# Kernel tuning notes

Hardware: AMD Instinct MI355X
Metric: run time of the kernel (lower is better)

The kernel has to match this reference:

```python
import jax, jax.numpy as jnp
import numpy as np

T, B, I, H, O = 512, 128, 512, 1024, 256

def setup_inputs() -> dict:
    key = jax.random.key(0)
    ks = jax.random.split(key, 7)
    s = 1.0 / np.sqrt(H)
    return {
        "seqs": jax.random.normal(ks[0], (T, B, I), dtype=jnp.float32),
        "W_ih": jax.random.uniform(ks[1], (H, I), minval=-s, maxval=s, dtype=jnp.float32),
        "W_hh": jax.random.uniform(ks[2], (H, H), minval=-s, maxval=s, dtype=jnp.float32),
        "b_ih": jax.random.uniform(ks[3], (H,), minval=-s, maxval=s, dtype=jnp.float32),
        "b_hh": jax.random.uniform(ks[4], (H,), minval=-s, maxval=s, dtype=jnp.float32),
        "W_fc": jax.random.uniform(ks[5], (O, H), minval=-s, maxval=s, dtype=jnp.float32),
        "b_fc": jax.random.uniform(ks[6], (O,), minval=-s, maxval=s, dtype=jnp.float32),
    }

def reference(seqs, W_ih, W_hh, b_ih, b_hh, W_fc, b_fc):
    # Precompute input projections for all timesteps in one big GEMM: [T,B,H]
    x_proj = jnp.einsum('tbi,hi->tbh', seqs, W_ih) + b_ih + b_hh

    def step(h, xp):
        h_new = jax.nn.relu(xp + h @ W_hh.T)
        return h_new, None

    h0 = jnp.zeros((seqs.shape[1], W_hh.shape[0]), dtype=seqs.dtype)
    h_final, _ = jax.lax.scan(step, h0, x_proj)
    return h_final @ W_fc.T + b_fc
```

## Files before the change

### kernel.cpp

```cpp
#include <hip/hip_runtime.h>
#include <hip/hip_bf16.h>
#include <stdint.h>

#define T_STEPS 512
#define BATCH   128
#define IN      512
#define HID     1024
#define OUTN    256

typedef __bf16 bf16x8 __attribute__((ext_vector_type(8)));
typedef float  f32x4  __attribute__((ext_vector_type(4)));
typedef unsigned short us8 __attribute__((ext_vector_type(8)));
typedef unsigned int   ui4 __attribute__((ext_vector_type(4)));

#define TAGM 0x80008000u
#define CLRM 0x7FFF7FFFu

__device__ __forceinline__ unsigned short f2bf(float f) {
    uint32_t u = __float_as_uint(f);
    uint32_t r = (u + 0x7fffu + ((u >> 16) & 1u)) >> 16;
    return (unsigned short)r;
}

__device__ __forceinline__ ui4 ld_u128_agent(const void* p) {
    ui4 v;
    asm volatile("global_load_dwordx4 %0, %1, off sc0 sc1"
                 : "=v"(v) : "v"(p) : "memory");
    return v;
}

__device__ __forceinline__ bf16x8 ld_frag(const unsigned short* smem, int row, int kbyte, int rowstride) {
    int off = row * rowstride + (kbyte ^ ((row & 7) << 4));
    return *reinterpret_cast<const bf16x8*>(reinterpret_cast<const char*>(smem) + off);
}
__device__ __forceinline__ us8 ld_frag_u(const unsigned short* smem, int row, int kbyte, int rowstride) {
    int off = row * rowstride + (kbyte ^ ((row & 7) << 4));
    return *reinterpret_cast<const us8*>(reinterpret_cast<const char*>(smem) + off);
}

__global__ __launch_bounds__(256, 1) void rnn_persistent(
    const float* __restrict__ seqs, const float* __restrict__ W_ih,
    const float* __restrict__ W_hh, const float* __restrict__ b_ih,
    const float* __restrict__ b_hh, const float* __restrict__ W_fc,
    const float* __restrict__ b_fc, float* __restrict__ out,
    unsigned short* __restrict__ hbuf)
{
    const int tid  = threadIdx.x;
    const int lane = tid & 63;
    const int wv   = tid >> 6;
    const int wg   = blockIdx.x;
    const int g    = wg >> 5;
    const int w    = wg & 31;
    const int gr0  = g * 16;
    const int c0   = w * 32;
    const int ln15 = lane & 15;
    const int lk   = lane >> 4;

    __shared__ unsigned short xtile[16 * 512];
    __shared__ unsigned short htile[16 * 1024];
    __shared__ float red[4][16][33];
    __shared__ float biasS[32];

    bf16x8 wih[2][4];
    bf16x8 whh[2][8];
    #pragma unroll
    for (int nt = 0; nt < 2; nt++) {
        const int j = c0 + nt * 16 + ln15;
        #pragma unroll
        for (int s = 0; s < 4; s++) {
            const int k = wv * 128 + s * 32 + lk * 8;
            const float* p = W_ih + j * IN + k;
            us8 u;
            #pragma unroll
            for (int e = 0; e < 8; e++) u[e] = f2bf(p[e]);
            wih[nt][s] = __builtin_bit_cast(bf16x8, u);
        }
        #pragma unroll
        for (int s = 0; s < 8; s++) {
            const int k = wv * 256 + s * 32 + lk * 8;
            const float* p = W_hh + j * HID + k;
            us8 u;
            #pragma unroll
            for (int e = 0; e < 8; e++) u[e] = f2bf(p[e]);
            whh[nt][s] = __builtin_bit_cast(bf16x8, u);
        }
    }
    if (tid < 32) biasS[tid] = b_ih[c0 + tid] + b_hh[c0 + tid];

    int hgoff[8], hloff[8];
    #pragma unroll
    for (int it = 0; it < 8; it++) {
        const int c    = tid + it * 256;
        const int row  = c >> 7;
        const int colc = c & 127;
        hgoff[it] = row * 2048 + colc * 16;
        hloff[it] = row * 2048 + ((colc * 16) ^ ((row & 7) << 4));
    }

    const int xrow[4] = { (tid) >> 6, (tid + 256) >> 6, (tid + 512) >> 6, (tid + 768) >> 6 };
    const int xcol[4] = { (tid) & 63, (tid + 256) & 63, (tid + 512) & 63, (tid + 768) & 63 };

    us8 xbf[4];
    {
        const float* xsrc = seqs + (size_t)gr0 * IN;
        #pragma unroll
        for (int it = 0; it < 4; it++) {
            const float* s4 = xsrc + xrow[it] * IN + xcol[it] * 8;
            float4 a = *reinterpret_cast<const float4*>(s4);
            float4 b = *reinterpret_cast<const float4*>(s4 + 4);
            us8 u;
            u[0]=f2bf(a.x); u[1]=f2bf(a.y); u[2]=f2bf(a.z); u[3]=f2bf(a.w);
            u[4]=f2bf(b.x); u[5]=f2bf(b.y); u[6]=f2bf(b.z); u[7]=f2bf(b.w);
            xbf[it] = u;
        }
    }

    const size_t slotB = (size_t)BATCH * HID * 2;
    char* hbase = reinterpret_cast<char*>(hbuf);

    for (int t = 0; t < T_STEPS; t++) {
        #pragma unroll
        for (int it = 0; it < 4; it++) {
            const int off = xrow[it] * 1024 + ((xcol[it] * 16) ^ ((xrow[it] & 7) << 4));
            *reinterpret_cast<us8*>(reinterpret_cast<char*>(xtile) + off) = xbf[it];
        }
        __syncthreads();

        ui4 hv[8];
        const char* hsrc = hbase + (size_t)(t & 1) * slotB + (size_t)gr0 * HID * 2;
        if (t > 0) {
            #pragma unroll
            for (int it = 0; it < 8; it++) hv[it] = ld_u128_agent(hsrc + hgoff[it]);
        }
        __builtin_amdgcn_sched_barrier(0);

        float4 xr[8];
        {
            const int tn = (t + 1 < T_STEPS) ? t + 1 : t;
            const float* xsrc = seqs + (size_t)tn * (BATCH * IN) + (size_t)gr0 * IN;
            #pragma unroll
            for (int it = 0; it < 4; it++) {
                const float* s4 = xsrc + xrow[it] * IN + xcol[it] * 8;
                xr[2*it]   = *reinterpret_cast<const float4*>(s4);
                xr[2*it+1] = *reinterpret_cast<const float4*>(s4 + 4);
            }
        }
        __builtin_amdgcn_sched_barrier(0);

        f32x4 acc0 = {0.f, 0.f, 0.f, 0.f};
        f32x4 acc1 = {0.f, 0.f, 0.f, 0.f};
        {
            const int kx0b = wv * 256;
            #pragma unroll
            for (int s = 0; s < 4; s++) {
                bf16x8 a = ld_frag(xtile, ln15, kx0b + s * 64 + lk * 16, 1024);
                acc0 = __builtin_amdgcn_mfma_f32_16x16x32_bf16(a, wih[0][s], acc0, 0, 0, 0);
                acc1 = __builtin_amdgcn_mfma_f32_16x16x32_bf16(a, wih[1][s], acc1, 0, 0, 0);
            }
        }

        if (t > 0) {
            const unsigned pr = ((t >> 1) & 1) ? 0x80000000u : 0x00008000u;
            asm volatile("s_waitcnt vmcnt(8)" ::: "memory");
            __builtin_amdgcn_sched_barrier(0);
            unsigned pending = 0xFFu;
            while (true) {
                unsigned np = 0;
                #pragma unroll
                for (int it = 0; it < 8; it++) {
                    if (pending & (1u << it)) {
                        unsigned d = ((hv[it][0] & TAGM) ^ pr) | ((hv[it][1] & TAGM) ^ pr)
                                   | ((hv[it][2] & TAGM) ^ pr) | ((hv[it][3] & TAGM) ^ pr);
                        if (d != 0u) {
                            np |= (1u << it);
                            hv[it] = ld_u128_agent(hsrc + hgoff[it]);
                        }
                    }
                }
                pending = np;
                if (pending == 0u) break;
                asm volatile("s_waitcnt vmcnt(0)" ::: "memory");
                __builtin_amdgcn_sched_barrier(0);
            }
            #pragma unroll
            for (int it = 0; it < 8; it++) {
                ui4 v = hv[it];
                v[0] &= CLRM; v[1] &= CLRM; v[2] &= CLRM; v[3] &= CLRM;
                *reinterpret_cast<ui4*>(reinterpret_cast<char*>(htile) + hloff[it]) = v;
            }
            __syncthreads();

            const int kh0b = wv * 512;
            #pragma unroll
            for (int s = 0; s < 8; s++) {
                bf16x8 a = ld_frag(htile, ln15, kh0b + s * 64 + lk * 16, 2048);
                acc0 = __builtin_amdgcn_mfma_f32_16x16x32_bf16(a, whh[0][s], acc0, 0, 0, 0);
                acc1 = __builtin_amdgcn_mfma_f32_16x16x32_bf16(a, whh[1][s], acc1, 0, 0, 0);
            }
        }

        #pragma unroll
        for (int r = 0; r < 4; r++) {
            red[wv][lk * 4 + r][ln15]      = acc0[r];
            red[wv][lk * 4 + r][16 + ln15] = acc1[r];
        }
        __syncthreads();
        const int hrow = tid >> 4;
        const int co2  = (tid & 15) * 2;
        float v0 = red[0][hrow][co2]   + red[1][hrow][co2]   + red[2][hrow][co2]   + red[3][hrow][co2]   + biasS[co2];
        float v1 = red[0][hrow][co2+1] + red[1][hrow][co2+1] + red[2][hrow][co2+1] + red[3][hrow][co2+1] + biasS[co2+1];
        v0 = fmaxf(v0, 0.0f);
        v1 = fmaxf(v1, 0.0f);

        asm volatile("s_waitcnt vmcnt(0)" ::: "memory");
        __builtin_amdgcn_sched_barrier(0);
        #pragma unroll
        for (int it = 0; it < 4; it++) {
            float4 a = xr[2*it], b = xr[2*it+1];
            us8 u;
            u[0]=f2bf(a.x); u[1]=f2bf(a.y); u[2]=f2bf(a.z); u[3]=f2bf(a.w);
            u[4]=f2bf(b.x); u[5]=f2bf(b.y); u[6]=f2bf(b.z); u[7]=f2bf(b.w);
            xbf[it] = u;
        }

        {
            const unsigned pw = (((t + 1) >> 1) & 1) ? 0x80000000u : 0x00008000u;
            unsigned pack = (unsigned)f2bf(v0) | ((unsigned)f2bf(v1) << 16) | pw;
            unsigned* dst = reinterpret_cast<unsigned*>(
                hbase + (size_t)((t + 1) & 1) * slotB
                + ((size_t)(gr0 + hrow) * HID + c0 + co2) * 2);
            __hip_atomic_store(dst, pack, __ATOMIC_RELAXED, __HIP_MEMORY_SCOPE_AGENT);
        }
    }

    {
        const char* hsrc = hbase + (size_t)gr0 * HID * 2;
        ui4 hv[8];
        #pragma unroll
        for (int it = 0; it < 8; it++) hv[it] = ld_u128_agent(hsrc + hgoff[it]);
        unsigned pending = 0xFFu;
        do {
            asm volatile("s_waitcnt vmcnt(0)" ::: "memory");
            __builtin_amdgcn_sched_barrier(0);
            unsigned np = 0;
            #pragma unroll
            for (int it = 0; it < 8; it++) {
                if (pending & (1u << it)) {
                    unsigned d = ((hv[it][0] & TAGM) ^ 0x00008000u) | ((hv[it][1] & TAGM) ^ 0x00008000u)
                               | ((hv[it][2] & TAGM) ^ 0x00008000u) | ((hv[it][3] & TAGM) ^ 0x00008000u);
                    if (d != 0u) {
                        np |= (1u << it);
                        hv[it] = ld_u128_agent(hsrc + hgoff[it]);
                    }
                }
            }
            pending = np;
        } while (pending);
        #pragma unroll
        for (int it = 0; it < 8; it++) {
            ui4 v = hv[it];
            v[0] &= CLRM; v[1] &= CLRM; v[2] &= CLRM; v[3] &= CLRM;
            *reinterpret_cast<ui4*>(reinterpret_cast<char*>(htile) + hloff[it]) = v;
        }
        __syncthreads();
    }

    {
        const int oi   = tid & 127;
        const int half = tid >> 7;
        const int row  = oi >> 3;
        const int o    = w * 8 + (oi & 7);
        const float* wf = W_fc + (size_t)o * HID + half * 512;
        float sum = 0.f;
        #pragma unroll 4
        for (int ck = 0; ck < 64; ck++) {
            us8 hu = ld_frag_u(htile, row, half * 1024 + ck * 16, 2048);
            float4 wa = *reinterpret_cast<const float4*>(wf + ck * 8);
            float4 wb = *reinterpret_cast<const float4*>(wf + ck * 8 + 4);
            sum += __uint_as_float((unsigned)hu[0] << 16) * wa.x
                 + __uint_as_float((unsigned)hu[1] << 16) * wa.y
                 + __uint_as_float((unsigned)hu[2] << 16) * wa.z
                 + __uint_as_float((unsigned)hu[3] << 16) * wa.w
                 + __uint_as_float((unsigned)hu[4] << 16) * wb.x
                 + __uint_as_float((unsigned)hu[5] << 16) * wb.y
                 + __uint_as_float((unsigned)hu[6] << 16) * wb.z
                 + __uint_as_float((unsigned)hu[7] << 16) * wb.w;
        }
        float* redf = &red[0][0][0];
        redf[tid] = sum;
        __syncthreads();
        if (tid < 128) {
            out[(size_t)(gr0 + row) * OUTN + o] = redf[tid] + redf[tid + 128] + b_fc[o];
        }
    }
}

extern "C" void kernel_launch(void* const* d_in, const int* in_sizes, int n_in,
                              void* d_out, int out_size, void* d_ws, size_t ws_size,
                              hipStream_t stream) {
    const float* seqs = (const float*)d_in[0];
    const float* W_ih = (const float*)d_in[1];
    const float* W_hh = (const float*)d_in[2];
    const float* b_ih = (const float*)d_in[3];
    const float* b_hh = (const float*)d_in[4];
    const float* W_fc = (const float*)d_in[5];
    const float* b_fc = (const float*)d_in[6];
    float* out = (float*)d_out;

    unsigned short* hbuf = (unsigned short*)d_ws;

    hipMemsetAsync(hbuf, 0, 2 * BATCH * HID * sizeof(unsigned short), stream);
    rnn_persistent<<<dim3(256), dim3(256), 0, stream>>>(
        seqs, W_ih, W_hh, b_ih, b_hh, W_fc, b_fc, out, hbuf);
}
```

Measured before the change: 1.594 ms.

## Halve workgroup count and add per-group step flags before polling hidden state

Restructures the persistent RNN kernel from 256 blocks of 256 threads to 128 blocks of 512 threads. Each block now covers 64 hidden columns, using two column halves of four K-split waves. A per-block flag array is added: each block publishes its completed step after storing its slice of h, and consumers spin on the 16 flags of their batch group before loading h. This replaces repeated tagged-data polling of 8 loads per thread, intended to cut cross-block traffic and the number of participants per group barrier. The cost is extra syncthreads, a vmcnt(0) wait plus flag store on every step, and larger blocks with fewer CUs in use.

```diff
diff --git a/kernel.cpp b/kernel.cpp
--- a/kernel.cpp
+++ b/kernel.cpp
@@ -38,37 +38,40 @@
     return *reinterpret_cast<const us8*>(reinterpret_cast<const char*>(smem) + off);
 }
 
-__global__ __launch_bounds__(256, 1) void rnn_persistent(
+__global__ __launch_bounds__(512, 1) void rnn_persistent(
     const float* __restrict__ seqs, const float* __restrict__ W_ih,
     const float* __restrict__ W_hh, const float* __restrict__ b_ih,
     const float* __restrict__ b_hh, const float* __restrict__ W_fc,
     const float* __restrict__ b_fc, float* __restrict__ out,
-    unsigned short* __restrict__ hbuf)
+    unsigned short* __restrict__ hbuf,
+    unsigned int* __restrict__ flags)
 {
-    const int tid  = threadIdx.x;
-    const int lane = tid & 63;
-    const int wv   = tid >> 6;
-    const int wg   = blockIdx.x;
-    const int g    = wg >> 5;
-    const int w    = wg & 31;
-    const int gr0  = g * 16;
-    const int c0   = w * 32;
-    const int ln15 = lane & 15;
-    const int lk   = lane >> 4;
+    const int tid   = threadIdx.x;
+    const int lane  = tid & 63;
+    const int wv    = tid >> 6;
+    const int kteam = wv & 3;
+    const int chalf = wv >> 2;
+    const int wg    = blockIdx.x;
+    const int g     = wg >> 4;
+    const int w     = wg & 15;
+    const int gr0   = g * 16;
+    const int c0    = w * 64;
+    const int ln15  = lane & 15;
+    const int lk    = lane >> 4;
 
     __shared__ unsigned short xtile[16 * 512];
     __shared__ unsigned short htile[16 * 1024];
-    __shared__ float red[4][16][33];
-    __shared__ float biasS[32];
+    __shared__ float red[4][16][66];
+    __shared__ float biasS[64];
 
     bf16x8 wih[2][4];
     bf16x8 whh[2][8];
     #pragma unroll
     for (int nt = 0; nt < 2; nt++) {
-        const int j = c0 + nt * 16 + ln15;
+        const int j = c0 + chalf * 32 + nt * 16 + ln15;
         #pragma unroll
         for (int s = 0; s < 4; s++) {
-            const int k = wv * 128 + s * 32 + lk * 8;
+            const int k = kteam * 128 + s * 32 + lk * 8;
             const float* p = W_ih + j * IN + k;
             us8 u;
             #pragma unroll
@@ -77,7 +80,7 @@
         }
         #pragma unroll
         for (int s = 0; s < 8; s++) {
-            const int k = wv * 256 + s * 32 + lk * 8;
+            const int k = kteam * 256 + s * 32 + lk * 8;
             const float* p = W_hh + j * HID + k;
             us8 u;
             #pragma unroll
@@ -85,26 +88,29 @@
             whh[nt][s] = __builtin_bit_cast(bf16x8, u);
         }
     }
-    if (tid < 32) biasS[tid] = b_ih[c0 + tid] + b_hh[c0 + tid];
-
-    int hgoff[8], hloff[8];
+    if (tid < 64) biasS[tid] = b_ih[c0 + tid] + b_hh[c0 + tid];
+
+    unsigned int* grp_flags = flags + g * 16;
+    unsigned int* my_flag   = grp_flags + w;
+
+    int hgoff[4], hloff[4];
     #pragma unroll
-    for (int it = 0; it < 8; it++) {
-        const int c    = tid + it * 256;
+    for (int it = 0; it < 4; it++) {
+        const int c    = tid + it * 512;
         const int row  = c >> 7;
         const int colc = c & 127;
         hgoff[it] = row * 2048 + colc * 16;
         hloff[it] = row * 2048 + ((colc * 16) ^ ((row & 7) << 4));
     }
 
-    const int xrow[4] = { (tid) >> 6, (tid + 256) >> 6, (tid + 512) >> 6, (tid + 768) >> 6 };
-    const int xcol[4] = { (tid) & 63, (tid + 256) & 63, (tid + 512) & 63, (tid + 768) & 63 };
-
-    us8 xbf[4];
+    const int xrow[2] = { (tid) >> 6, (tid + 512) >> 6 };
+    const int xcol[2] = { (tid) & 63, (tid + 512) & 63 };
+
+    us8 xbf[2];
     {
         const float* xsrc = seqs + (size_t)gr0 * IN;
         #pragma unroll
-        for (int it = 0; it < 4; it++) {
+        for (int it = 0; it < 2; it++) {
             const float* s4 = xsrc + xrow[it] * IN + xcol[it] * 8;
             float4 a = *reinterpret_cast<const float4*>(s4);
             float4 b = *reinterpret_cast<const float4*>(s4 + 4);
@@ -119,27 +125,26 @@
     char* hbase = reinterpret_cast<char*>(hbuf);
 
     for (int t = 0; t < T_STEPS; t++) {
-        #pragma unroll
-        for (int it = 0; it < 4; it++) {
+        ui4 hv[4];
+        const char* hsrc = hbase + (size_t)(t & 1) * slotB + (size_t)gr0 * HID * 2;
+        if (t > 0) {
+            #pragma unroll
+            for (int it = 0; it < 4; it++) hv[it] = ld_u128_agent(hsrc + hgoff[it]);
+        }
+        __builtin_amdgcn_sched_barrier(0);
+
+        #pragma unroll
+        for (int it = 0; it < 2; it++) {
             const int off = xrow[it] * 1024 + ((xcol[it] * 16) ^ ((xrow[it] & 7) << 4));
             *reinterpret_cast<us8*>(reinterpret_cast<char*>(xtile) + off) = xbf[it];
         }
-        __syncthreads();
-
-        ui4 hv[8];
-        const char* hsrc = hbase + (size_t)(t & 1) * slotB + (size_t)gr0 * HID * 2;
-        if (t > 0) {
-            #pragma unroll
-            for (int it = 0; it < 8; it++) hv[it] = ld_u128_agent(hsrc + hgoff[it]);
-        }
-        __builtin_amdgcn_sched_barrier(0);
-
-        float4 xr[8];
+
+        float4 xr[4];
         {
             const int tn = (t + 1 < T_STEPS) ? t + 1 : t;
             const float* xsrc = seqs + (size_t)tn * (BATCH * IN) + (size_t)gr0 * IN;
             #pragma unroll
-            for (int it = 0; it < 4; it++) {
+            for (int it = 0; it < 2; it++) {
                 const float* s4 = xsrc + xrow[it] * IN + xcol[it] * 8;
                 xr[2*it]   = *reinterpret_cast<const float4*>(s4);
                 xr[2*it+1] = *reinterpret_cast<const float4*>(s4 + 4);
@@ -147,10 +152,16 @@
         }
         __builtin_amdgcn_sched_barrier(0);
 
+        if (t > 0 && wv == 0 && lane < 16) {
+            const unsigned int* f = grp_flags + lane;
+            while (__hip_atomic_load(f, __ATOMIC_RELAXED, __HIP_MEMORY_SCOPE_AGENT) < (unsigned)t) { }
+        }
+        __syncthreads();
+
         f32x4 acc0 = {0.f, 0.f, 0.f, 0.f};
         f32x4 acc1 = {0.f, 0.f, 0.f, 0.f};
         {
-            const int kx0b = wv * 256;
+            const int kx0b = kteam * 256;
             #pragma unroll
             for (int s = 0; s < 4; s++) {
                 bf16x8 a = ld_frag(xtile, ln15, kx0b + s * 64 + lk * 16, 1024);
@@ -161,13 +172,13 @@
 
         if (t > 0) {
             const unsigned pr = ((t >> 1) & 1) ? 0x80000000u : 0x00008000u;
-            asm volatile("s_waitcnt vmcnt(8)" ::: "memory");
+            asm volatile("s_waitcnt vmcnt(4)" ::: "memory");
             __builtin_amdgcn_sched_barrier(0);
-            unsigned pending = 0xFFu;
+            unsigned pending = 0xFu;
             while (true) {
                 unsigned np = 0;
                 #pragma unroll
-                for (int it = 0; it < 8; it++) {
+                for (int it = 0; it < 4; it++) {
                     if (pending & (1u << it)) {
                         unsigned d = ((hv[it][0] & TAGM) ^ pr) | ((hv[it][1] & TAGM) ^ pr)
                                    | ((hv[it][2] & TAGM) ^ pr) | ((hv[it][3] & TAGM) ^ pr);
@@ -183,14 +194,14 @@
                 __builtin_amdgcn_sched_barrier(0);
             }
             #pragma unroll
-            for (int it = 0; it < 8; it++) {
+            for (int it = 0; it < 4; it++) {
                 ui4 v = hv[it];
                 v[0] &= CLRM; v[1] &= CLRM; v[2] &= CLRM; v[3] &= CLRM;
                 *reinterpret_cast<ui4*>(reinterpret_cast<char*>(htile) + hloff[it]) = v;
             }
             __syncthreads();
 
-            const int kh0b = wv * 512;
+            const int kh0b = kteam * 512;
             #pragma unroll
             for (int s = 0; s < 8; s++) {
                 bf16x8 a = ld_frag(htile, ln15, kh0b + s * 64 + lk * 16, 2048);
@@ -201,29 +212,18 @@
 
         #pragma unroll
         for (int r = 0; r < 4; r++) {
-            red[wv][lk * 4 + r][ln15]      = acc0[r];
-            red[wv][lk * 4 + r][16 + ln15] = acc1[r];
-        }
-        __syncthreads();
-        const int hrow = tid >> 4;
-        const int co2  = (tid & 15) * 2;
-        float v0 = red[0][hrow][co2]   + red[1][hrow][co2]   + red[2][hrow][co2]   + red[3][hrow][co2]   + biasS[co2];
-        float v1 = red[0][hrow][co2+1] + red[1][hrow][co2+1] + red[2][hrow][co2+1] + red[3][hrow][co2+1] + biasS[co2+1];
-        v0 = fmaxf(v0, 0.0f);
-        v1 = fmaxf(v1, 0.0f);
-
-        asm volatile("s_waitcnt vmcnt(0)" ::: "memory");
-        __builtin_amdgcn_sched_barrier(0);
-        #pragma unroll
-        for (int it = 0; it < 4; it++) {
-            float4 a = xr[2*it], b = xr[2*it+1];
-            us8 u;
-            u[0]=f2bf(a.x); u[1]=f2bf(a.y); u[2]=f2bf(a.z); u[3]=f2bf(a.w);
-            u[4]=f2bf(b.x); u[5]=f2bf(b.y); u[6]=f2bf(b.z); u[7]=f2bf(b.w);
-            xbf[it] = u;
-        }
-
+            red[kteam][lk * 4 + r][chalf * 32 + ln15]      = acc0[r];
+            red[kteam][lk * 4 + r][chalf * 32 + 16 + ln15] = acc1[r];
+        }
+        __syncthreads();
         {
+            const int hrow = tid >> 5;
+            const int co2  = (tid & 31) * 2;
+            float v0 = red[0][hrow][co2]   + red[1][hrow][co2]   + red[2][hrow][co2]   + red[3][hrow][co2]   + biasS[co2];
+            float v1 = red[0][hrow][co2+1] + red[1][hrow][co2+1] + red[2][hrow][co2+1] + red[3][hrow][co2+1] + biasS[co2+1];
+            v0 = fmaxf(v0, 0.0f);
+            v1 = fmaxf(v1, 0.0f);
+
             const unsigned pw = (((t + 1) >> 1) & 1) ? 0x80000000u : 0x00008000u;
             unsigned pack = (unsigned)f2bf(v0) | ((unsigned)f2bf(v1) << 16) | pw;
             unsigned* dst = reinterpret_cast<unsigned*>(
@@ -231,20 +231,41 @@
                 + ((size_t)(gr0 + hrow) * HID + c0 + co2) * 2);
             __hip_atomic_store(dst, pack, __ATOMIC_RELAXED, __HIP_MEMORY_SCOPE_AGENT);
         }
+        asm volatile("s_waitcnt vmcnt(0)" ::: "memory");
+        __builtin_amdgcn_sched_barrier(0);
+        __syncthreads();
+        if (tid == 0) {
+            __hip_atomic_store(my_flag, (unsigned)(t + 1), __ATOMIC_RELAXED, __HIP_MEMORY_SCOPE_AGENT);
+        }
+
+        #pragma unroll
+        for (int it = 0; it < 2; it++) {
+            float4 a = xr[2*it], b = xr[2*it+1];
+            us8 u;
+            u[0]=f2bf(a.x); u[1]=f2bf(a.y); u[2]=f2bf(a.z); u[3]=f2bf(a.w);
+            u[4]=f2bf(b.x); u[5]=f2bf(b.y); u[6]=f2bf(b.z); u[7]=f2bf(b.w);
+            xbf[it] = u;
+        }
     }
 
     {
         const char* hsrc = hbase + (size_t)gr0 * HID * 2;
-        ui4 hv[8];
-        #pragma unroll
-        for (int it = 0; it < 8; it++) hv[it] = ld_u128_agent(hsrc + hgoff[it]);
-        unsigned pending = 0xFFu;
-        do {
-            asm volatile("s_waitcnt vmcnt(0)" ::: "memory");
-            __builtin_amdgcn_sched_barrier(0);
+        ui4 hv[4];
+        #pragma unroll
+        for (int it = 0; it < 4; it++) hv[it] = ld_u128_agent(hsrc + hgoff[it]);
+        __builtin_amdgcn_sched_barrier(0);
+        if (wv == 0 && lane < 16) {
+            const unsigned int* f = grp_flags + lane;
+            while (__hip_atomic_load(f, __ATOMIC_RELAXED, __HIP_MEMORY_SCOPE_AGENT) < (unsigned)T_STEPS) { }
+        }
+        __syncthreads();
+        asm volatile("s_waitcnt vmcnt(0)" ::: "memory");
+        __builtin_amdgcn_sched_barrier(0);
+        unsigned pending = 0xFu;
+        while (true) {
             unsigned np = 0;
             #pragma unroll
-            for (int it = 0; it < 8; it++) {
+            for (int it = 0; it < 4; it++) {
                 if (pending & (1u << it)) {
                     unsigned d = ((hv[it][0] & TAGM) ^ 0x00008000u) | ((hv[it][1] & TAGM) ^ 0x00008000u)
                                | ((hv[it][2] & TAGM) ^ 0x00008000u) | ((hv[it][3] & TAGM) ^ 0x00008000u);
@@ -255,9 +276,12 @@
                 }
             }
             pending = np;
-        } while (pending);
-        #pragma unroll
-        for (int it = 0; it < 8; it++) {
+            if (pending == 0u) break;
+            asm volatile("s_waitcnt vmcnt(0)" ::: "memory");
+            __builtin_amdgcn_sched_barrier(0);
+        }
+        #pragma unroll
+        for (int it = 0; it < 4; it++) {
             ui4 v = hv[it];
             v[0] &= CLRM; v[1] &= CLRM; v[2] &= CLRM; v[3] &= CLRM;
             *reinterpret_cast<ui4*>(reinterpret_cast<char*>(htile) + hloff[it]) = v;
@@ -266,10 +290,10 @@
     }
 
     {
-        const int oi   = tid & 127;
-        const int half = tid >> 7;
-        const int row  = oi >> 3;
-        const int o    = w * 8 + (oi & 7);
+        const int oi   = tid & 255;
+        const int half = tid >> 8;
+        const int row  = oi >> 4;
+        const int o    = w * 16 + (oi & 15);
         const float* wf = W_fc + (size_t)o * HID + half * 512;
         float sum = 0.f;
         #pragma unroll 4
@@ -289,8 +313,9 @@
         float* redf = &red[0][0][0];
         redf[tid] = sum;
         __syncthreads();
-        if (tid < 128) {
-            out[(size_t)(gr0 + row) * OUTN + o] = redf[tid] + redf[tid + 128] + b_fc[o];
+        if (tid < 256) {
+            out[(size_t)(gr0 + (tid >> 4)) * OUTN + w * 16 + (tid & 15)] =
+                redf[tid] + redf[tid + 256] + b_fc[w * 16 + (tid & 15)];
         }
     }
 }
@@ -307,9 +332,11 @@
     const float* b_fc = (const float*)d_in[6];
     float* out = (float*)d_out;
 
-    unsigned short* hbuf = (unsigned short*)d_ws;
-
-    hipMemsetAsync(hbuf, 0, 2 * BATCH * HID * sizeof(unsigned short), stream);
-    rnn_persistent<<<dim3(256), dim3(256), 0, stream>>>(
-        seqs, W_ih, W_hh, b_ih, b_hh, W_fc, b_fc, out, hbuf);
-}
+    char* ws = (char*)d_ws;
+    unsigned short* hbuf  = (unsigned short*)ws;
+    unsigned int*   flags = (unsigned int*)(ws + 524288);
+
+    hipMemsetAsync(ws, 0, 524288 + 512, stream);
+    rnn_persistent<<<dim3(128), dim3(512), 0, stream>>>(
+        seqs, W_ih, W_hh, b_ih, b_hh, W_fc, b_fc, out, hbuf, flags);
+}
```

New measurement: 1.840 ms. +15.4%, slower.

## Gate hidden-state reads on per-workgroup step-counter flags before loading

Applied to the files above, without the earlier changes.

Adds a per-group array of step counters that each workgroup bumps after writing its slice of the hidden state. Before loading h, one wave spins on its group's 32 flags, and the loads then follow a barrier. This replaces the old approach of polling tag bits on the data itself from the start and reissuing loads until they match. The aim is to avoid repeated 128-bit reloads of the hidden tile and contention on the data lines. The cost is a serialized flag wait plus barrier on the critical path, and the flag store is relaxed with no release ordering, so the tag check is kept as a fallback.

```diff
diff --git a/kernel.cpp b/kernel.cpp
--- a/kernel.cpp
+++ b/kernel.cpp
@@ -43,7 +43,8 @@
     const float* __restrict__ W_hh, const float* __restrict__ b_ih,
     const float* __restrict__ b_hh, const float* __restrict__ W_fc,
     const float* __restrict__ b_fc, float* __restrict__ out,
-    unsigned short* __restrict__ hbuf)
+    unsigned short* __restrict__ hbuf,
+    unsigned int* __restrict__ flags)
 {
     const int tid  = threadIdx.x;
     const int lane = tid & 63;
@@ -87,6 +88,9 @@
     }
     if (tid < 32) biasS[tid] = b_ih[c0 + tid] + b_hh[c0 + tid];
 
+    unsigned int* grp_flags = flags + g * 32;
+    unsigned int* my_flag   = grp_flags + w;
+
     int hgoff[8], hloff[8];
     #pragma unroll
     for (int it = 0; it < 8; it++) {
@@ -124,15 +128,6 @@
             const int off = xrow[it] * 1024 + ((xcol[it] * 16) ^ ((xrow[it] & 7) << 4));
             *reinterpret_cast<us8*>(reinterpret_cast<char*>(xtile) + off) = xbf[it];
         }
-        __syncthreads();
-
-        ui4 hv[8];
-        const char* hsrc = hbase + (size_t)(t & 1) * slotB + (size_t)gr0 * HID * 2;
-        if (t > 0) {
-            #pragma unroll
-            for (int it = 0; it < 8; it++) hv[it] = ld_u128_agent(hsrc + hgoff[it]);
-        }
-        __builtin_amdgcn_sched_barrier(0);
 
         float4 xr[8];
         {
@@ -145,6 +140,19 @@
                 xr[2*it+1] = *reinterpret_cast<const float4*>(s4 + 4);
             }
         }
+
+        if (t > 0 && wv == 0 && lane < 32) {
+            const unsigned int* f = grp_flags + lane;
+            while (__hip_atomic_load(f, __ATOMIC_RELAXED, __HIP_MEMORY_SCOPE_AGENT) < (unsigned)t) { }
+        }
+        __syncthreads();
+
+        ui4 hv[8];
+        const char* hsrc = hbase + (size_t)(t & 1) * slotB + (size_t)gr0 * HID * 2;
+        if (t > 0) {
+            #pragma unroll
+            for (int it = 0; it < 8; it++) hv[it] = ld_u128_agent(hsrc + hgoff[it]);
+        }
         __builtin_amdgcn_sched_barrier(0);
 
         f32x4 acc0 = {0.f, 0.f, 0.f, 0.f};
@@ -161,7 +169,7 @@
 
         if (t > 0) {
             const unsigned pr = ((t >> 1) & 1) ? 0x80000000u : 0x00008000u;
-            asm volatile("s_waitcnt vmcnt(8)" ::: "memory");
+            asm volatile("s_waitcnt vmcnt(0)" ::: "memory");
             __builtin_amdgcn_sched_barrier(0);
             unsigned pending = 0xFFu;
             while (true) {
@@ -205,23 +213,13 @@
             red[wv][lk * 4 + r][16 + ln15] = acc1[r];
         }
         __syncthreads();
+
         const int hrow = tid >> 4;
         const int co2  = (tid & 15) * 2;
         float v0 = red[0][hrow][co2]   + red[1][hrow][co2]   + red[2][hrow][co2]   + red[3][hrow][co2]   + biasS[co2];
         float v1 = red[0][hrow][co2+1] + red[1][hrow][co2+1] + red[2][hrow][co2+1] + red[3][hrow][co2+1] + biasS[co2+1];
         v0 = fmaxf(v0, 0.0f);
         v1 = fmaxf(v1, 0.0f);
-
-        asm volatile("s_waitcnt vmcnt(0)" ::: "memory");
-        __builtin_amdgcn_sched_barrier(0);
-        #pragma unroll
-        for (int it = 0; it < 4; it++) {
-            float4 a = xr[2*it], b = xr[2*it+1];
-            us8 u;
-            u[0]=f2bf(a.x); u[1]=f2bf(a.y); u[2]=f2bf(a.z); u[3]=f2bf(a.w);
-            u[4]=f2bf(b.x); u[5]=f2bf(b.y); u[6]=f2bf(b.z); u[7]=f2bf(b.w);
-            xbf[it] = u;
-        }
 
         {
             const unsigned pw = (((t + 1) >> 1) & 1) ? 0x80000000u : 0x00008000u;
@@ -231,17 +229,37 @@
                 + ((size_t)(gr0 + hrow) * HID + c0 + co2) * 2);
             __hip_atomic_store(dst, pack, __ATOMIC_RELAXED, __HIP_MEMORY_SCOPE_AGENT);
         }
+
+        if (tid == 0) {
+            __hip_atomic_store(my_flag, (unsigned)(t + 1), __ATOMIC_RELAXED, __HIP_MEMORY_SCOPE_AGENT);
+        }
+
+        asm volatile("s_waitcnt vmcnt(0)" ::: "memory");
+        __builtin_amdgcn_sched_barrier(0);
+        #pragma unroll
+        for (int it = 0; it < 4; it++) {
+            float4 a = xr[2*it], b = xr[2*it+1];
+            us8 u;
+            u[0]=f2bf(a.x); u[1]=f2bf(a.y); u[2]=f2bf(a.z); u[3]=f2bf(a.w);
+            u[4]=f2bf(b.x); u[5]=f2bf(b.y); u[6]=f2bf(b.z); u[7]=f2bf(b.w);
+            xbf[it] = u;
+        }
     }
 
     {
+        if (wv == 0 && lane < 32) {
+            const unsigned int* f = grp_flags + lane;
+            while (__hip_atomic_load(f, __ATOMIC_RELAXED, __HIP_MEMORY_SCOPE_AGENT) < (unsigned)T_STEPS) { }
+        }
+        __syncthreads();
         const char* hsrc = hbase + (size_t)gr0 * HID * 2;
         ui4 hv[8];
         #pragma unroll
         for (int it = 0; it < 8; it++) hv[it] = ld_u128_agent(hsrc + hgoff[it]);
+        asm volatile("s_waitcnt vmcnt(0)" ::: "memory");
+        __builtin_amdgcn_sched_barrier(0);
         unsigned pending = 0xFFu;
-        do {
-            asm volatile("s_waitcnt vmcnt(0)" ::: "memory");
-            __builtin_amdgcn_sched_barrier(0);
+        while (true) {
             unsigned np = 0;
             #pragma unroll
             for (int it = 0; it < 8; it++) {
@@ -255,7 +273,10 @@
                 }
             }
             pending = np;
-        } while (pending);
+            if (pending == 0u) break;
+            asm volatile("s_waitcnt vmcnt(0)" ::: "memory");
+            __builtin_amdgcn_sched_barrier(0);
+        }
         #pragma unroll
         for (int it = 0; it < 8; it++) {
             ui4 v = hv[it];
@@ -307,9 +328,11 @@
     const float* b_fc = (const float*)d_in[6];
     float* out = (float*)d_out;
 
-    unsigned short* hbuf = (unsigned short*)d_ws;
-
-    hipMemsetAsync(hbuf, 0, 2 * BATCH * HID * sizeof(unsigned short), stream);
+    char* ws = (char*)d_ws;
+    unsigned short* hbuf  = (unsigned short*)ws;
+    unsigned int*   flags = (unsigned int*)(ws + 524288);
+
+    hipMemsetAsync(ws, 0, 524288 + 1024, stream);
     rnn_persistent<<<dim3(256), dim3(256), 0, stream>>>(
-        seqs, W_ih, W_hh, b_ih, b_hh, W_fc, b_fc, out, hbuf);
-}
+        seqs, W_ih, W_hh, b_ih, b_hh, W_fc, b_fc, out, hbuf, flags);
+}
```

Result: no change. 1.566 ms (-1.8%).
